# Performance work log

Hardware: AMD Instinct MI355X
Metric: run time of the kernel (lower is better)

Reference implementation:

```python
import jax, jax.numpy as jnp
import numpy as np

IN_DIM, OUT_DIM, NUM_KNOTS = 256, 256, 20
X_MIN, X_MAX = -5.0, 5.0
H = (X_MAX - X_MIN) / (NUM_KNOTS - 1)  # uniform knot spacing


def setup_inputs() -> dict:
    key = jax.random.key(0)
    k1, k2 = jax.random.split(key, 2)
    x = jax.random.normal(k1, (1024, IN_DIM), dtype=jnp.float32) * 2.0
    # per-(out,in)-pair cubic coefficients for each of the NUM_KNOTS-1 intervals: [a,b,c,d]
    coeffs = jax.random.normal(k2, (OUT_DIM, IN_DIM, NUM_KNOTS - 1, 4), dtype=jnp.float32) * 0.1
    bias = jnp.zeros((OUT_DIM,), dtype=jnp.float32)
    return {"x": x, "coeffs": coeffs, "bias": bias}


def reference(x, coeffs, bias):
    # x: [B, I]; coeffs: [J, I, K, 4]; bias: [J]
    B, I = x.shape
    K = coeffs.shape[2]
    # locate knot interval (clamped -> linear-cubic extrapolation at edges)
    idx = jnp.clip(jnp.floor((x - X_MIN) / H).astype(jnp.int32), 0, K - 1)  # [B, I]
    t = x - (X_MIN + idx.astype(x.dtype) * H)                               # [B, I]
    # gather per-pair interval coefficients: [J, B, I, 4]
    i_arr = jnp.broadcast_to(jnp.arange(I)[None, :], idx.shape)
    c = coeffs[:, i_arr, idx]
    a, b, c2, d = c[..., 0], c[..., 1], c[..., 2], c[..., 3]
    # Horner evaluation; t broadcasts [B,I] -> [J,B,I]
    y = ((d * t + c2) * t + b) * t + a
    # sum over input dims, add bias: [B, J]
    return y.sum(axis=-1).T + bias[None, :]
```

## Files before the change

### kernel.cpp

```cpp
#include <hip/hip_runtime.h>

#define IN_DIM   256
#define OUT_DIM  256
#define NKNOT    19
#define NCOL     (IN_DIM * NKNOT)
#define CPQ      1216
#define SLICE_U4 (CPQ * 32 * 2)
#define X_MIN_C  (-5.0f)
#define H_C      (10.0f / 19.0f)
#define INV_H_C  (19.0f / 10.0f)

__device__ __forceinline__ unsigned int pk_bf16(float x, float y) {
    unsigned int ux = __float_as_uint(x); ux += 0x7FFFu + ((ux >> 16) & 1u);
    unsigned int uy = __float_as_uint(y); uy += 0x7FFFu + ((uy >> 16) & 1u);
    return (ux >> 16) | (uy & 0xFFFF0000u);
}
__device__ __forceinline__ float lo16(unsigned int u) { return __uint_as_float(u << 16); }
__device__ __forceinline__ float hi16(unsigned int u) { return __uint_as_float(u & 0xFFFF0000u); }

__global__ __launch_bounds__(256) void transpose_pack(
        const float4* __restrict__ src, uint4* __restrict__ dst) {
    __shared__ float4 tile[64][65];
    const int c0 = (blockIdx.x % 76) * 64;
    const int r0 = (blockIdx.x / 76) * 64;
    const int tx = threadIdx.x & 63;
    const int ty = threadIdx.x >> 6;

    #pragma unroll
    for (int jj = 0; jj < 16; ++jj) {
        const int r = ty * 16 + jj;
        tile[tx][r] = src[(size_t)(r0 + r) * NCOL + (size_t)(c0 + tx)];
    }
    __syncthreads();

    const int quarter = c0 / CPQ;
    const int clbase  = c0 - quarter * CPQ;
    const int o_half  = r0 >> 7;
    const int og_base = (r0 & 127) >> 2;
    uint4* base = dst + (size_t)(quarter * 2 + o_half) * SLICE_U4;

    #pragma unroll
    for (int jj = 0; jj < 4; ++jj) {
        const int p  = jj * 256 + threadIdx.x;
        const int cl = p >> 4;
        const int og = p & 15;
        const float4 v0 = tile[cl][og * 4 + 0];
        const float4 v1 = tile[cl][og * 4 + 1];
        const float4 v2 = tile[cl][og * 4 + 2];
        const float4 v3 = tile[cl][og * 4 + 3];
        uint4 ab, cd;
        ab.x = pk_bf16(v0.x, v1.x); ab.y = pk_bf16(v2.x, v3.x);
        ab.z = pk_bf16(v0.y, v1.y); ab.w = pk_bf16(v2.y, v3.y);
        cd.x = pk_bf16(v0.z, v1.z); cd.y = pk_bf16(v2.z, v3.z);
        cd.z = pk_bf16(v0.w, v1.w); cd.w = pk_bf16(v2.w, v3.w);
        const size_t e = ((size_t)(clbase + cl) * 32 + (og_base + og)) * 2;
        base[e]     = ab;
        base[e + 1] = cd;
    }
}

__global__ __launch_bounds__(256, 4) void kan_partial(
        const float* __restrict__ x,
        const uint4* __restrict__ Ct,
        float4*      __restrict__ part,
        int n4q) {
    __shared__ int2 s_tk[8 * 64];

    const int s       = blockIdx.x & 7;
    const int o_half  = s & 1;
    const int quarter = s >> 1;
    const int bgrp    = blockIdx.x >> 3;
    const int tid     = threadIdx.x;

    {
        const int col = tid & 63;
        const int row = tid >> 6;
        #pragma unroll
        for (int bs = row; bs < 8; bs += 4) {
            const float xv = x[(bgrp * 8 + bs) * IN_DIM + quarter * 64 + col];
            const float f  = (xv - X_MIN_C) * INV_H_C;
            int idx = (int)floorf(f);
            idx = idx < 0 ? 0 : (idx > NKNOT - 1 ? NKNOT - 1 : idx);
            s_tk[bs * 64 + col] =
                make_int2(idx * 64, __float_as_int(xv - (X_MIN_C + (float)idx * H_C)));
        }
    }
    __syncthreads();

    const int og = tid & 31;
    const int bs = tid >> 5;
    const uint4* base = Ct + (size_t)s * SLICE_U4 + og * 2;
    const int2* tkp = s_tk + bs * 64;

    float y0 = 0.f, y1 = 0.f, y2 = 0.f, y3 = 0.f;

    #pragma unroll 4
    for (int ii = 0; ii < 64; ++ii) {
        const int2 tk = tkp[ii];
        const int  e  = ii * 1216 + tk.x;
        const uint4 AB = base[e];
        const uint4 CD = base[e + 1];
        const float t  = __int_as_float(tk.y);
        const float a_0 = lo16(AB.x), a_1 = hi16(AB.x), a_2 = lo16(AB.y), a_3 = hi16(AB.y);
        const float b_0 = lo16(AB.z), b_1 = hi16(AB.z), b_2 = lo16(AB.w), b_3 = hi16(AB.w);
        const float c_0 = lo16(CD.x), c_1 = hi16(CD.x), c_2 = lo16(CD.y), c_3 = hi16(CD.y);
        const float d_0 = lo16(CD.z), d_1 = hi16(CD.z), d_2 = lo16(CD.w), d_3 = hi16(CD.w);
        y0 += ((d_0 * t + c_0) * t + b_0) * t + a_0;
        y1 += ((d_1 * t + c_1) * t + b_1) * t + a_1;
        y2 += ((d_2 * t + c_2) * t + b_2) * t + a_2;
        y3 += ((d_3 * t + c_3) * t + b_3) * t + a_3;
    }

    const int b = bgrp * 8 + bs;
    part[(size_t)quarter * n4q + (size_t)b * 64 + (o_half * 32 + og)] =
        make_float4(y0, y1, y2, y3);
}

__global__ __launch_bounds__(256) void kan_reduce(
        const float4* __restrict__ part,
        const float4* __restrict__ bias4,
        float4*       __restrict__ out,
        int n4) {
    const int n = blockIdx.x * 256 + threadIdx.x;
    if (n < n4) {
        const float4 p0 = part[n];
        const float4 p1 = part[n4 + n];
        const float4 p2 = part[2 * n4 + n];
        const float4 p3 = part[3 * n4 + n];
        const float4 bv = bias4[n & 63];
        float4 r;
        r.x = (p0.x + p1.x) + (p2.x + p3.x) + bv.x;
        r.y = (p0.y + p1.y) + (p2.y + p3.y) + bv.y;
        r.z = (p0.z + p1.z) + (p2.z + p3.z) + bv.z;
        r.w = (p0.w + p1.w) + (p2.w + p3.w) + bv.w;
        out[n] = r;
    }
}

extern "C" void kernel_launch(void* const* d_in, const int* in_sizes, int n_in,
                              void* d_out, int out_size, void* d_ws, size_t ws_size,
                              hipStream_t stream) {
    const float* x      = (const float*)d_in[0];
    const float* coeffs = (const float*)d_in[1];
    const float* bias   = (const float*)d_in[2];
    float*       out    = (float*)d_out;

    const int B = in_sizes[0] / IN_DIM;
    uint4* Ct   = (uint4*)d_ws;
    float* part = (float*)((char*)d_ws + (16u << 20));

    transpose_pack<<<304, 256, 0, stream>>>((const float4*)coeffs, Ct);

    const int n4 = B * OUT_DIM / 4;
    kan_partial<<<B, 256, 0, stream>>>(x, Ct, (float4*)part, n4);
    kan_reduce<<<(n4 + 255) / 256, 256, 0, stream>>>(
        (const float4*)part, (const float4*)bias, (float4*)out, n4);
}
```

Baseline: 100.3 us.

## Switch coefficients to fp16 and evaluate cubic as fdot2 against packed t powers

```diff
diff --git a/kernel.cpp b/kernel.cpp
--- a/kernel.cpp
+++ b/kernel.cpp
@@ -5,22 +5,31 @@
 #define NKNOT    19
 #define NCOL     (IN_DIM * NKNOT)
 #define CPQ      1216
-#define SLICE_U4 (CPQ * 32 * 2)
+#define SLICE_U4 (CPQ * 64)
 #define X_MIN_C  (-5.0f)
 #define H_C      (10.0f / 19.0f)
 #define INV_H_C  (19.0f / 10.0f)
 
-__device__ __forceinline__ unsigned int pk_bf16(float x, float y) {
-    unsigned int ux = __float_as_uint(x); ux += 0x7FFFu + ((ux >> 16) & 1u);
-    unsigned int uy = __float_as_uint(y); uy += 0x7FFFu + ((uy >> 16) & 1u);
-    return (ux >> 16) | (uy & 0xFFFF0000u);
+typedef __fp16 half2_t __attribute__((ext_vector_type(2)));
+
+__device__ __forceinline__ unsigned int pk_f16(float x, float y) {
+    return __builtin_bit_cast(unsigned int, __builtin_amdgcn_cvt_pkrtz(x, y));
 }
-__device__ __forceinline__ float lo16(unsigned int u) { return __uint_as_float(u << 16); }
-__device__ __forceinline__ float hi16(unsigned int u) { return __uint_as_float(u & 0xFFFF0000u); }
+
+__device__ __forceinline__ float fdot2(unsigned int w, unsigned int c, float acc) {
+#if __has_builtin(__builtin_amdgcn_fdot2)
+    return __builtin_amdgcn_fdot2(__builtin_bit_cast(half2_t, w),
+                                  __builtin_bit_cast(half2_t, c), acc, false);
+#else
+    half2_t a = __builtin_bit_cast(half2_t, w);
+    half2_t b = __builtin_bit_cast(half2_t, c);
+    return acc + (float)a.x * (float)b.x + (float)a.y * (float)b.y;
+#endif
+}
 
 __global__ __launch_bounds__(256) void transpose_pack(
         const float4* __restrict__ src, uint4* __restrict__ dst) {
-    __shared__ float4 tile[64][65];
+    __shared__ uint2 tile[64][65];
     const int c0 = (blockIdx.x % 76) * 64;
     const int r0 = (blockIdx.x / 76) * 64;
     const int tx = threadIdx.x & 63;
@@ -29,42 +38,38 @@
     #pragma unroll
     for (int jj = 0; jj < 16; ++jj) {
         const int r = ty * 16 + jj;
-        tile[tx][r] = src[(size_t)(r0 + r) * NCOL + (size_t)(c0 + tx)];
+        const float4 v = src[(size_t)(r0 + r) * NCOL + (size_t)(c0 + tx)];
+        uint2 p;
+        p.x = pk_f16(v.x, v.y);
+        p.y = pk_f16(v.z, v.w);
+        tile[tx][r] = p;
     }
     __syncthreads();
 
-    const int quarter = c0 / CPQ;
-    const int clbase  = c0 - quarter * CPQ;
-    const int o_half  = r0 >> 7;
-    const int og_base = (r0 & 127) >> 2;
+    const int quarter  = c0 / CPQ;
+    const int clbase   = c0 - quarter * CPQ;
+    const int o_half   = r0 >> 7;
+    const int og2_base = (r0 & 127) >> 1;
     uint4* base = dst + (size_t)(quarter * 2 + o_half) * SLICE_U4;
 
     #pragma unroll
-    for (int jj = 0; jj < 4; ++jj) {
-        const int p  = jj * 256 + threadIdx.x;
-        const int cl = p >> 4;
-        const int og = p & 15;
-        const float4 v0 = tile[cl][og * 4 + 0];
-        const float4 v1 = tile[cl][og * 4 + 1];
-        const float4 v2 = tile[cl][og * 4 + 2];
-        const float4 v3 = tile[cl][og * 4 + 3];
-        uint4 ab, cd;
-        ab.x = pk_bf16(v0.x, v1.x); ab.y = pk_bf16(v2.x, v3.x);
-        ab.z = pk_bf16(v0.y, v1.y); ab.w = pk_bf16(v2.y, v3.y);
-        cd.x = pk_bf16(v0.z, v1.z); cd.y = pk_bf16(v2.z, v3.z);
-        cd.z = pk_bf16(v0.w, v1.w); cd.w = pk_bf16(v2.w, v3.w);
-        const size_t e = ((size_t)(clbase + cl) * 32 + (og_base + og)) * 2;
-        base[e]     = ab;
-        base[e + 1] = cd;
+    for (int jj = 0; jj < 8; ++jj) {
+        const int p     = jj * 256 + threadIdx.x;
+        const int cl    = p >> 5;
+        const int og2l  = p & 31;
+        const uint2 t0  = tile[cl][og2l * 2];
+        const uint2 t1  = tile[cl][og2l * 2 + 1];
+        base[(size_t)(clbase + cl) * 64 + og2_base + og2l] =
+            make_uint4(t0.x, t0.y, t1.x, t1.y);
     }
 }
 
 __global__ __launch_bounds__(256, 4) void kan_partial(
         const float* __restrict__ x,
         const uint4* __restrict__ Ct,
-        float4*      __restrict__ part,
-        int n4q) {
-    __shared__ int2 s_tk[8 * 64];
+        float2*      __restrict__ part,
+        int B) {
+    __shared__ int4 s_tk[4 * 64];
 
     const int s       = blockIdx.x & 7;
     const int o_half  = s & 1;
@@ -74,46 +79,42 @@
 
     {
         const int col = tid & 63;
-        const int row = tid >> 6;
-        #pragma unroll
-        for (int bs = row; bs < 8; bs += 4) {
-            const float xv = x[(bgrp * 8 + bs) * IN_DIM + quarter * 64 + col];
-            const float f  = (xv - X_MIN_C) * INV_H_C;
-            int idx = (int)floorf(f);
-            idx = idx < 0 ? 0 : (idx > NKNOT - 1 ? NKNOT - 1 : idx);
-            s_tk[bs * 64 + col] =
-                make_int2(idx * 64, __float_as_int(xv - (X_MIN_C + (float)idx * H_C)));
-        }
+        const int bs  = tid >> 6;
+        const float xv = x[(bgrp * 4 + bs) * IN_DIM + quarter * 64 + col];
+        const float f  = (xv - X_MIN_C) * INV_H_C;
+        int idx = (int)floorf(f);
+        idx = idx < 0 ? 0 : (idx > NKNOT - 1 ? NKNOT - 1 : idx);
+        const float t  = xv - (X_MIN_C + (float)idx * H_C);
+        const float t2 = t * t;
+        const float t3 = t2 * t;
+        s_tk[bs * 64 + col] = make_int4(idx * 64,
+                                        (int)pk_f16(1.0f, t),
+                                        (int)pk_f16(t2, t3), 0);
     }
     __syncthreads();
 
-    const int og = tid & 31;
-    const int bs = tid >> 5;
-    const uint4* base = Ct + (size_t)s * SLICE_U4 + og * 2;
-    const int2* tkp = s_tk + bs * 64;
+    const int og2 = tid & 63;
+    const int bs  = tid >> 6;
+    const uint4* base = Ct + (size_t)s * SLICE_U4;
+    const int4* tkp = s_tk + bs * 64;
 
-    float y0 = 0.f, y1 = 0.f, y2 = 0.f, y3 = 0.f;
+    float y0 = 0.f, y1 = 0.f;
 
-    #pragma unroll 4
+    #pragma unroll 8
     for (int ii = 0; ii < 64; ++ii) {
-        const int2 tk = tkp[ii];
-        const int  e  = ii * 1216 + tk.x;
-        const uint4 AB = base[e];
-        const uint4 CD = base[e + 1];
-        const float t  = __int_as_float(tk.y);
-        const float a_0 = lo16(AB.x), a_1 = hi16(AB.x), a_2 = lo16(AB.y), a_3 = hi16(AB.y);
-        const float b_0 = lo16(AB.z), b_1 = hi16(AB.z), b_2 = lo16(AB.w), b_3 = hi16(AB.w);
-        const float c_0 = lo16(CD.x), c_1 = hi16(CD.x), c_2 = lo16(CD.y), c_3 = hi16(CD.y);
-        const float d_0 = lo16(CD.z), d_1 = hi16(CD.z), d_2 = lo16(CD.w), d_3 = hi16(CD.w);
-        y0 += ((d_0 * t + c_0) * t + b_0) * t + a_0;
-        y1 += ((d_1 * t + c_1) * t + b_1) * t + a_1;
-        y2 += ((d_2 * t + c_2) * t + b_2) * t + a_2;
-        y3 += ((d_3 * t + c_3) * t + b_3) * t + a_3;
+        const int4 tk = tkp[ii];
+        const uint4 Q = base[og2 + ii * 1216 + tk.x];
+        const unsigned int w01 = (unsigned int)tk.y;
+        const unsigned int w23 = (unsigned int)tk.z;
+        y0 = fdot2(w01, Q.x, y0);
+        y0 = fdot2(w23, Q.y, y0);
+        y1 = fdot2(w01, Q.z, y1);
+        y1 = fdot2(w23, Q.w, y1);
     }
 
-    const int b = bgrp * 8 + bs;
-    part[(size_t)quarter * n4q + (size_t)b * 64 + (o_half * 32 + og)] =
-        make_float4(y0, y1, y2, y3);
+    const int b = bgrp * 4 + bs;
+    part[(size_t)quarter * (B * 128) + (size_t)b * 128 + o_half * 64 + og2] =
+        make_float2(y0, y1);
 }
 
 __global__ __launch_bounds__(256) void kan_reduce(
@@ -151,8 +152,9 @@
 
     transpose_pack<<<304, 256, 0, stream>>>((const float4*)coeffs, Ct);
 
+    kan_partial<<<(B / 4) * 8, 256, 0, stream>>>(x, Ct, (float2*)part, B);
+
     const int n4 = B * OUT_DIM / 4;
-    kan_partial<<<B, 256, 0, stream>>>(x, Ct, (float4*)part, n4);
     kan_reduce<<<(n4 + 255) / 256, 256, 0, stream>>>(
         (const float4*)part, (const float4*)bias, (float4*)out, n4);
 }
```

Result: faster. 93.76 us (-6.5%).
